# Performance work log

Measured on AMD Instinct MI355X. Metric: run time of the kernel, lower is better.

## Reference

```python
import jax, jax.numpy as jnp
from jax import lax
import numpy as np

THRESHOLD = 1.25
CURRENT_DECAY = 0.25
VOLTAGE_DECAY = 0.03
TAU_GRAD = 0.03
SCALE_GRAD = 3.0


@jax.custom_vjp
def spike_fn(v):
    # Heaviside spike on membrane voltage (threshold already subtracted)
    return (v >= 0.0).astype(v.dtype)

def _spike_fwd(v):
    return spike_fn(v), v

def _spike_bwd(v, g):
    # slayer-style exponential surrogate gradient around threshold
    surrogate = SCALE_GRAD * jnp.exp(-jnp.abs(v) / TAU_GRAD)
    return (g * surrogate,)

spike_fn.defvjp(_spike_fwd, _spike_bwd)


def cuba_dense(x, v_w, g_w, delay):
    """x: [B, C_in, T] spikes -> [B, C_out, T] spikes.
    Weight-normalized dense synapse + CUBA leaky-integrate-and-fire scan + axonal delay."""
    # weight norm: W = g * v / ||v||_row
    norm = jnp.sqrt(jnp.sum(v_w * v_w, axis=1, keepdims=True))
    W = g_w[:, None] * v_w / norm                       # [O, C]
    z = jnp.einsum('bct,oc->bot', x, W)                 # synaptic current input [B, O, T]
    B, O, T = z.shape
    zT = jnp.transpose(z, (2, 0, 1))                    # [T, B, O]

    def step(carry, zt):
        cur, vol = carry
        cur = cur * (1.0 - CURRENT_DECAY) + zt
        vol = vol * (1.0 - VOLTAGE_DECAY) + cur
        s = spike_fn(vol - THRESHOLD)
        vol = vol * (1.0 - s)                           # reset to zero on spike
        return (cur, vol), s

    init = (jnp.zeros((B, O), z.dtype), jnp.zeros((B, O), z.dtype))
    _, sT = lax.scan(step, init, zT)                    # [T, B, O]
    s = jnp.transpose(sT, (1, 2, 0))                    # [B, O, T]

    # per-neuron integer axonal delay: out[b,n,t] = s[b,n,t-d_n]
    t_idx = jnp.arange(T)[None, :] - delay[:, None]     # [O, T]
    valid = (t_idx >= 0)
    gathered = s[:, jnp.arange(O)[:, None], jnp.clip(t_idx, 0, T - 1)]
    return jnp.where(valid[None, :, :], gathered, jnp.zeros((), s.dtype))


def setup_inputs() -> dict:
    key = jax.random.key(0)
    ks = jax.random.split(key, 10)
    B, C, T = 32, 34 * 34 * 2, 300
    spike = (jax.random.uniform(ks[0], (B, C, T)) < 0.1).astype(jnp.float32)
    v1 = jax.random.normal(ks[1], (512, C), jnp.float32) * 0.1
    g1 = jax.random.uniform(ks[2], (512,), jnp.float32) + 0.5
    v2 = jax.random.normal(ks[3], (512, 512), jnp.float32) * 0.1
    g2 = jax.random.uniform(ks[4], (512,), jnp.float32) + 0.5
    v3 = jax.random.normal(ks[5], (10, 512), jnp.float32) * 0.1
    g3 = jax.random.uniform(ks[6], (10,), jnp.float32) + 0.5
    d1 = jax.random.randint(ks[7], (512,), 0, 8, jnp.int32)
    d2 = jax.random.randint(ks[8], (512,), 0, 8, jnp.int32)
    d3 = jax.random.randint(ks[9], (10,), 0, 8, jnp.int32)
    return {"spike": spike, "v1": v1, "g1": g1, "v2": v2, "g2": g2,
            "v3": v3, "g3": g3, "d1": d1, "d2": d2, "d3": d3}


def reference(spike, v1, g1, v2, g2, v3, g3, d1, d2, d3):
    s1 = cuba_dense(spike, v1, g1, d1)
    s2 = cuba_dense(s1, v2, g2, d2)
    s3 = cuba_dense(s2, v3, g3, d3)
    counts = jnp.stack([jnp.mean(s1), jnp.mean(s2), jnp.mean(s3)]).reshape(1, -1)
    return s3, counts
```

## Files before the change

kernel.cpp:

```cpp
#include <hip/hip_runtime.h>

#define B_   32
#define T_   300
#define C1_  2312
#define O1_  512
#define O2_  512
#define O3_  10
#define M_   (B_*T_)
#define KSPLIT_ 1152


__global__ void calc_f(const float* __restrict__ v, const float* __restrict__ g,
                       double* __restrict__ f, int O, int C) {
    int o = blockIdx.x;
    const float* row = v + (size_t)o * C;
    double s = 0.0;
    for (int c = threadIdx.x; c < C; c += blockDim.x) {
        double x = (double)row[c];
        s += x * x;
    }
    for (int off = 32; off; off >>= 1) s += __shfl_down(s, off);
    __shared__ double wsum[4];
    int lane = threadIdx.x & 63, wv = threadIdx.x >> 6;
    if (lane == 0) wsum[wv] = s;
    __syncthreads();
    if (threadIdx.x == 0) {
        double tot = 0.0;
        for (int i = 0; i < (int)(blockDim.x >> 6); ++i) tot += wsum[i];
        f[o] = (double)g[o] / sqrt(tot);
    }
}

__global__ void transpose_scale(const float* __restrict__ v, const double* __restrict__ f,
                                double* __restrict__ wt, int O, int C, int ldo) {
    __shared__ double tile[32][33];
    int c0 = blockIdx.x * 32, o0 = blockIdx.y * 32;
    int tx = threadIdx.x, ty = threadIdx.y;
    for (int k = 0; k < 4; ++k) {
        int o = o0 + ty + k * 8, c = c0 + tx;
        double val = 0.0;
        if (o < O && c < C) val = (double)v[(size_t)o * C + c] * f[o];
        tile[ty + k * 8][tx] = val;
    }
    __syncthreads();
    for (int k = 0; k < 4; ++k) {
        int c = c0 + ty + k * 8, o = o0 + tx;
        if (c < C && o < O) wt[(size_t)c * ldo + o] = tile[tx][ty + k * 8];
    }
}

__global__ void build_bits(const float* __restrict__ X, unsigned* __restrict__ bits) {
    size_t idx = (size_t)blockIdx.x * 256 + threadIdx.x;
    if (idx >= (size_t)B_ * C1_ * 10) return;
    int t32 = (int)(idx % 10);
    size_t bc = idx / 10;
    const float* src = X + bc * T_ + t32 * 32;
    int nq = (t32 == 9) ? 3 : 8;
    unsigned m = 0;
    for (int q = 0; q < nq; ++q) {
        float4 v = *(const float4*)(src + q * 4);
        if (v.x != 0.f) m |= 1u << (q * 4 + 0);
        if (v.y != 0.f) m |= 1u << (q * 4 + 1);
        if (v.z != 0.f) m |= 1u << (q * 4 + 2);
        if (v.w != 0.f) m |= 1u << (q * 4 + 3);
    }
    bits[idx] = m;
}

__global__ __launch_bounds__(512, 4) void gemm1(const unsigned* __restrict__ Xbits,
                                                const double* __restrict__ Wt,
                                                double* __restrict__ Z0,
                                                double* __restrict__ Z1) {
    __shared__ double Ws[2][16][256];
    int n = blockIdx.x;
    int combo = n & 3;
    int khalf = combo & 1;
    int o0 = (combo >> 1) * 256;
    int i = n >> 2;
    int tb = i % 10;
    int bpair = i / 10;
    int tid = threadIdx.x;
    int w = tid >> 6;
    int lane = tid & 63;
    int b = bpair * 2 + (w >> 2);
    int w8s = __builtin_amdgcn_readfirstlane((w & 3) << 3);
    int cbeg = khalf ? KSPLIT_ : 0;
    int qend = khalf ? C1_ : KSPLIT_;
    const int NT = khalf ? 73 : 72;
    double* __restrict__ Z = khalf ? Z1 : Z0;
    double acc[8][4];
#pragma unroll
    for (int tj = 0; tj < 8; ++tj)
#pragma unroll
        for (int i2 = 0; i2 < 4; ++i2) acc[tj][i2] = 0.0;
    const unsigned* xbp = Xbits + (size_t)b * C1_ * 10 + tb;

    double2 wreg[4];
    unsigned mval, mvaln = 0u;

    auto load_w = [&](int c0) {
#pragma unroll
        for (int h = 0; h < 4; ++h) {
            int idx = h * 512 + tid;
            int r = idx >> 7, od = (idx & 127) * 2;
            int c = c0 + r;
            double2 val; val.x = 0.0; val.y = 0.0;
            if (c < qend) val = *(const double2*)(Wt + (size_t)c * O1_ + o0 + od);
            wreg[h] = val;
        }
    };
    auto load_m = [&](int c0) -> unsigned {
        int c = c0 + lane;
        return (lane < 16 && c < qend) ? xbp[(size_t)c * 10] : 0u;
    };
    auto store_w = [&](int bi) {
#pragma unroll
        for (int h = 0; h < 4; ++h) {
            int idx = h * 512 + tid;
            int r = idx >> 7, od = (idx & 127) * 2;
            *(double2*)(&Ws[bi][r][od]) = wreg[h];
        }
    };

    load_w(cbeg);
    mval = load_m(cbeg);
    store_w(0);
    __syncthreads();
    int cur = 0;
    for (int tile = 0; tile < NT; ++tile) {
        if (tile + 1 < NT) {
            int cn = cbeg + (tile + 1) * 16;
            load_w(cn);
            mvaln = load_m(cn);
        }
#pragma unroll
        for (int k = 0; k < 16; ++k) {
            unsigned smk = (unsigned)__builtin_amdgcn_readlane((int)mval, k);
            unsigned soct = (smk >> w8s) & 0xffu;
            if (soct) {
                double wf[4];
#pragma unroll
                for (int i2 = 0; i2 < 4; ++i2) wf[i2] = Ws[cur][k][lane + 64 * i2];
#pragma unroll
                for (int tj = 0; tj < 8; ++tj) {
                    if (soct & (1u << tj)) {
#pragma unroll
                        for (int i2 = 0; i2 < 4; ++i2) acc[tj][i2] += wf[i2];
                    }
                }
            }
        }
        if (tile + 1 < NT) {
            store_w(cur ^ 1);
            __syncthreads();
        }
        mval = mvaln;
        cur ^= 1;
    }
#pragma unroll
    for (int tj = 0; tj < 8; ++tj) {
        int t = tb * 32 + w8s + tj;
        if (t < T_) {
            double* dst = Z + ((size_t)b * T_ + t) * O1_ + o0;
#pragma unroll
            for (int i2 = 0; i2 < 4; ++i2)
                dst[lane + 64 * i2] = acc[tj][i2];
        }
    }
}

__global__ __launch_bounds__(512, 4) void gemm2s(const unsigned* __restrict__ Sbits,
                                                 const double* __restrict__ Wt,
                                                 double* __restrict__ Z0,
                                                 double* __restrict__ Z1) {
    __shared__ double Ws[2][16][256];
    int n = blockIdx.x;
    int combo = n & 3;
    int khalf = combo & 1;
    int o0 = (combo >> 1) * 256;
    int i = n >> 2;
    int twin = i % 5;
    int b = i / 5;
    int tid = threadIdx.x;
    int w = tid >> 6;
    int lane = tid & 63;
    int w8s = __builtin_amdgcn_readfirstlane((w & 3) << 3);
    int word = twin * 2 + (w >> 2);
    int cbeg = khalf * 256;
    double* __restrict__ Z = khalf ? Z1 : Z0;
    double acc[8][4];
#pragma unroll
    for (int tj = 0; tj < 8; ++tj)
#pragma unroll
        for (int i2 = 0; i2 < 4; ++i2) acc[tj][i2] = 0.0;
    const unsigned* xbp = Sbits + (size_t)b * O1_ * 10 + word;

    double2 wreg[4];
    unsigned mval, mvaln = 0u;

    auto load_w = [&](int c0) {
#pragma unroll
        for (int h = 0; h < 4; ++h) {
            int idx = h * 512 + tid;
            int r = idx >> 7, od = (idx & 127) * 2;
            int c = c0 + r;
            wreg[h] = *(const double2*)(Wt + (size_t)c * O2_ + o0 + od);
        }
    };
    auto load_m = [&](int c0) -> unsigned {
        int c = c0 + lane;
        return (lane < 16) ? xbp[(size_t)c * 10] : 0u;
    };
    auto store_w = [&](int bi) {
#pragma unroll
        for (int h = 0; h < 4; ++h) {
            int idx = h * 512 + tid;
            int r = idx >> 7, od = (idx & 127) * 2;
            *(double2*)(&Ws[bi][r][od]) = wreg[h];
        }
    };

    load_w(cbeg);
    mval = load_m(cbeg);
    store_w(0);
    __syncthreads();
    int cur = 0;
    for (int tile = 0; tile < 16; ++tile) {
        if (tile + 1 < 16) {
            int cn = cbeg + (tile + 1) * 16;
            load_w(cn);
            mvaln = load_m(cn);
        }
#pragma unroll
        for (int k = 0; k < 16; ++k) {
            unsigned smk = (unsigned)__builtin_amdgcn_readlane((int)mval, k);
            unsigned soct = (smk >> w8s) & 0xffu;
            if (soct) {
                double wf[4];
#pragma unroll
                for (int i2 = 0; i2 < 4; ++i2) wf[i2] = Ws[cur][k][lane + 64 * i2];
#pragma unroll
                for (int tj = 0; tj < 8; ++tj) {
                    if (soct & (1u << tj)) {
#pragma unroll
                        for (int i2 = 0; i2 < 4; ++i2) acc[tj][i2] += wf[i2];
                    }
                }
            }
        }
        if (tile + 1 < 16) {
            store_w(cur ^ 1);
            __syncthreads();
        }
        mval = mvaln;
        cur ^= 1;
    }
#pragma unroll
    for (int tj = 0; tj < 8; ++tj) {
        int t = twin * 64 + w * 8 + tj;
        if (t < T_) {
            double* dst = Z + ((size_t)b * T_ + t) * O2_ + o0;
#pragma unroll
            for (int i2 = 0; i2 < 4; ++i2)
                dst[lane + 64 * i2] = acc[tj][i2];
        }
    }
}

__global__ void gemm3(const float* __restrict__ A,
                      const double* __restrict__ Wt,
                      double* __restrict__ Z) {
    __shared__ double w[512 * 16];
    for (int e = threadIdx.x; e < 4096; e += 256)
        ((double2*)w)[e] = ((const double2*)Wt)[e];
    __syncthreads();
    int m = blockIdx.x * 256 + threadIdx.x;
    if (m >= M_) return;
    double acc[O3_];
#pragma unroll
    for (int o = 0; o < O3_; ++o) acc[o] = 0.0;
    const float4* Ar = (const float4*)(A + (size_t)m * 512);
    for (int cq = 0; cq < 128; ++cq) {
        float4 a = Ar[cq];
        float av[4] = {a.x, a.y, a.z, a.w};
#pragma unroll
        for (int u = 0; u < 4; ++u)
#pragma unroll
            for (int o = 0; o < O3_; ++o) acc[o] += (double)av[u] * w[(cq * 4 + u) * 16 + o];
    }
    double* dst = Z + (size_t)m * 16;
#pragma unroll
    for (int o = 0; o < O3_; ++o) dst[o] = acc[o];
}

__global__ void scan12(const double* __restrict__ Za,
                       const double* __restrict__ Zb,
                       const int* __restrict__ delay,
                       float* __restrict__ Sout,
                       unsigned* __restrict__ bitsOut,
                       float* __restrict__ sumOut) {
    int blk = blockIdx.x;
    int o = (blk & 7) * 64 + threadIdx.x;
    int b = blk >> 3;
    size_t base = (size_t)b * T_ * O1_ + o;
    const double* z  = Za + base;
    const double* z2 = Zb ? Zb + base : nullptr;
    float* s = Sout ? Sout + base : nullptr;
    int d = delay[o];
    if (s) for (int t = 0; t < d; ++t) s[(size_t)t * O1_] = 0.f;
    double cur = 0.0, vol = 0.0;
    float cnt = 0.f;
    unsigned bw = 0u;
    for (int t8 = 0; t8 < 296; t8 += 8) {
        double zbuf[8];
#pragma unroll
        for (int u = 0; u < 8; ++u) zbuf[u] = z[(size_t)(t8 + u) * O1_];
        if (z2) {
#pragma unroll
            for (int u = 0; u < 8; ++u) zbuf[u] += z2[(size_t)(t8 + u) * O1_];
        }
#pragma unroll
        for (int u = 0; u < 8; ++u) {
            int t = t8 + u;
            cur = cur * 0.75 + zbuf[u];
            vol = vol * 0.97 + cur;
            float sp = (vol >= 1.25) ? 1.f : 0.f;
            if (sp > 0.f) vol = 0.0;
            int tw = t + d;
            if (tw < T_) {
                if (s) s[(size_t)tw * O1_] = sp;
                cnt += sp;
                if (bitsOut) {
                    if (sp > 0.f) bw |= 1u << (tw & 31);
                    if ((tw & 31) == 31) { bitsOut[((size_t)b * O1_ + o) * 10 + (tw >> 5)] = bw; bw = 0u; }
                }
            }
        }
    }
    {
        double zbuf[4];
#pragma unroll
        for (int u = 0; u < 4; ++u) zbuf[u] = z[(size_t)(296 + u) * O1_];
        if (z2) {
#pragma unroll
            for (int u = 0; u < 4; ++u) zbuf[u] += z2[(size_t)(296 + u) * O1_];
        }
#pragma unroll
        for (int u = 0; u < 4; ++u) {
            int t = 296 + u;
            cur = cur * 0.75 + zbuf[u];
            vol = vol * 0.97 + cur;
            float sp = (vol >= 1.25) ? 1.f : 0.f;
            if (sp > 0.f) vol = 0.0;
            int tw = t + d;
            if (tw < T_) {
                if (s) s[(size_t)tw * O1_] = sp;
                cnt += sp;
                if (bitsOut) {
                    if (sp > 0.f) bw |= 1u << (tw & 31);
                    if ((tw & 31) == 31) { bitsOut[((size_t)b * O1_ + o) * 10 + (tw >> 5)] = bw; bw = 0u; }
                }
            }
        }
    }
    if (bitsOut) bitsOut[((size_t)b * O1_ + o) * 10 + 9] = bw;
    for (int off = 32; off; off >>= 1) cnt += __shfl_down(cnt, off);
    if (threadIdx.x == 0) atomicAdd(sumOut, cnt);
}

__global__ void scan3(const double* __restrict__ Z3,
                      const int* __restrict__ d3,
                      float* __restrict__ out,
                      float* __restrict__ sumOut) {
    __shared__ double zt[T_ * 16];
    int b = blockIdx.x;
    const double2* src = (const double2*)(Z3 + (size_t)b * T_ * 16);
    for (int e = threadIdx.x; e < T_ * 8; e += 64)
        ((double2*)zt)[e] = src[e];
    __syncthreads();
    int o = threadIdx.x;
    if (o < O3_) {
        int d = d3[o];
        float* dst = out + (size_t)b * O3_ * T_ + (size_t)o * T_;
        for (int t = 0; t < d; ++t) dst[t] = 0.f;
        double cur = 0.0, vol = 0.0;
        float cnt = 0.f;
        for (int t = 0; t < T_; ++t) {
            cur = cur * 0.75 + zt[t * 16 + o];
            vol = vol * 0.97 + cur;
            float sp = (vol >= 1.25) ? 1.f : 0.f;
            if (sp > 0.f) vol = 0.0;
            int tw = t + d;
            if (tw < T_) { dst[tw] = sp; cnt += sp; }
        }
        atomicAdd(sumOut, cnt);
    }
}

__global__ void finalize(const float* __restrict__ sums, float* __restrict__ out) {
    if (threadIdx.x == 0) {
        out[0] = (float)((double)sums[0] / (double)(B_ * O1_ * T_));
        out[1] = (float)((double)sums[1] / (double)(B_ * O2_ * T_));
        out[2] = (float)((double)sums[2] / (double)(B_ * O3_ * T_));
    }
}

extern "C" void kernel_launch(void* const* d_in, const int* in_sizes, int n_in,
                              void* d_out, int out_size, void* d_ws, size_t ws_size,
                              hipStream_t stream) {
    const float* spike = (const float*)d_in[0];
    const float* v1 = (const float*)d_in[1];
    const float* g1 = (const float*)d_in[2];
    const float* v2 = (const float*)d_in[3];
    const float* g2 = (const float*)d_in[4];
    const float* v3 = (const float*)d_in[5];
    const float* g3 = (const float*)d_in[6];
    const int* d1 = (const int*)d_in[7];
    const int* d2 = (const int*)d_in[8];
    const int* d3 = (const int*)d_in[9];
    float* out = (float*)d_out;

    double* dw = (double*)d_ws;
    size_t off = 0;
    double* f1  = dw + off; off += 512;
    double* f2  = dw + off; off += 512;
    double* f3  = dw + off; off += 16;
    double* Wt1 = dw + off; off += (size_t)C1_ * O1_;
    double* Wt2 = dw + off; off += 512 * 512;
    double* Wt3 = dw + off; off += 512 * 16;
    double* zA  = dw + off; off += (size_t)M_ * 512;
    double* zB  = dw + off; off += (size_t)M_ * 512;
    double* z3b = dw + off; off += (size_t)M_ * 16;
    float* fw = (float*)(dw + off);
    float* sB    = fw;
    float* sums  = fw + (size_t)M_ * 512;
    unsigned* Xbits = (unsigned*)(fw + (size_t)M_ * 512 + 4);
    unsigned* bits2 = Xbits + (size_t)B_ * C1_ * 10;
    (void)ws_size; (void)out_size; (void)in_sizes; (void)n_in;

    hipMemsetAsync(sums, 0, 4 * sizeof(float), stream);

    build_bits<<<(B_ * C1_ * 10 + 255) / 256, 256, 0, stream>>>(spike, Xbits);

    calc_f<<<512, 256, 0, stream>>>(v1, g1, f1, O1_, C1_);
    calc_f<<<512, 256, 0, stream>>>(v2, g2, f2, O2_, O1_);
    calc_f<<<O3_, 256, 0, stream>>>(v3, g3, f3, O3_, O2_);

    transpose_scale<<<dim3((C1_ + 31) / 32, 16), dim3(32, 8), 0, stream>>>(v1, f1, Wt1, O1_, C1_, O1_);
    transpose_scale<<<dim3(16, 16), dim3(32, 8), 0, stream>>>(v2, f2, Wt2, O2_, O1_, O2_);
    transpose_scale<<<dim3(16, 1), dim3(32, 8), 0, stream>>>(v3, f3, Wt3, O3_, O2_, 16);

    gemm1<<<640, 512, 0, stream>>>(Xbits, Wt1, zA, zB);
    scan12<<<256, 64, 0, stream>>>(zA, zB, d1, nullptr, bits2, sums + 0);
    gemm2s<<<640, 512, 0, stream>>>(bits2, Wt2, zA, zB);
    scan12<<<256, 64, 0, stream>>>(zA, zB, d2, sB, nullptr, sums + 1);
    gemm3<<<(M_ + 255) / 256, 256, 0, stream>>>(sB, Wt3, z3b);
    scan3<<<B_, 64, 0, stream>>>(z3b, d3, out, sums + 2);
    finalize<<<1, 64, 0, stream>>>(sums, out + (size_t)B_ * O3_ * T_);
}
```

Before: 794.1 us.

## Replace bit-packed sparse gemm2 with dense FP64 tiled FMA GEMM

Layer-2 GEMM previously used bit-packed spike masks and conditionally added weight rows only for active spikes, split over two K-halves. It now reads float spikes written by scan12 and runs a dense 32x128 tiled FP64 FMA GEMM over the full K. This removes the bit-packing, branch divergence and the second partial-sum buffer, but does full dense FP64 work regardless of spike sparsity. scan12 is now called with a null second buffer, so it must handle that case.

```diff
diff --git a/kernel.cpp b/kernel.cpp
--- a/kernel.cpp
+++ b/kernel.cpp
@@ -169,101 +169,53 @@
     }
 }
 
-__global__ __launch_bounds__(512, 4) void gemm2s(const unsigned* __restrict__ Sbits,
-                                                 const double* __restrict__ Wt,
-                                                 double* __restrict__ Z0,
-                                                 double* __restrict__ Z1) {
-    __shared__ double Ws[2][16][256];
-    int n = blockIdx.x;
-    int combo = n & 3;
-    int khalf = combo & 1;
-    int o0 = (combo >> 1) * 256;
-    int i = n >> 2;
-    int twin = i % 5;
-    int b = i / 5;
+__global__ __launch_bounds__(256, 4) void gemm2(const float* __restrict__ A,
+                                                const double* __restrict__ Wt,
+                                                double* __restrict__ Z) {
+    __shared__ double Ws[16][128];
+    __shared__ float  As[32][20];
+    int m0 = blockIdx.x * 32;
+    int o0 = blockIdx.y * 128;
     int tid = threadIdx.x;
-    int w = tid >> 6;
-    int lane = tid & 63;
-    int w8s = __builtin_amdgcn_readfirstlane((w & 3) << 3);
-    int word = twin * 2 + (w >> 2);
-    int cbeg = khalf * 256;
-    double* __restrict__ Z = khalf ? Z1 : Z0;
-    double acc[8][4];
-#pragma unroll
-    for (int tj = 0; tj < 8; ++tj)
-#pragma unroll
-        for (int i2 = 0; i2 < 4; ++i2) acc[tj][i2] = 0.0;
-    const unsigned* xbp = Sbits + (size_t)b * O1_ * 10 + word;
-
-    double2 wreg[4];
-    unsigned mval, mvaln = 0u;
-
-    auto load_w = [&](int c0) {
+    int to = tid & 31, tm = tid >> 5;
+    double acc[4][4];
+#pragma unroll
+    for (int i = 0; i < 4; ++i)
+#pragma unroll
+        for (int j = 0; j < 4; ++j) acc[i][j] = 0.0;
+    for (int c0 = 0; c0 < 512; c0 += 16) {
+        {
+            int r = tid >> 3, pr = tid & 7;
+            float2 v = *(const float2*)(A + (size_t)(m0 + r) * 512 + c0 + pr * 2);
+            As[r][pr * 2 + 0] = v.x;
+            As[r][pr * 2 + 1] = v.y;
+        }
 #pragma unroll
         for (int h = 0; h < 4; ++h) {
-            int idx = h * 512 + tid;
-            int r = idx >> 7, od = (idx & 127) * 2;
-            int c = c0 + r;
-            wreg[h] = *(const double2*)(Wt + (size_t)c * O2_ + o0 + od);
-        }
-    };
-    auto load_m = [&](int c0) -> unsigned {
-        int c = c0 + lane;
-        return (lane < 16) ? xbp[(size_t)c * 10] : 0u;
-    };
-    auto store_w = [&](int bi) {
-#pragma unroll
-        for (int h = 0; h < 4; ++h) {
-            int idx = h * 512 + tid;
-            int r = idx >> 7, od = (idx & 127) * 2;
-            *(double2*)(&Ws[bi][r][od]) = wreg[h];
-        }
-    };
-
-    load_w(cbeg);
-    mval = load_m(cbeg);
-    store_w(0);
-    __syncthreads();
-    int cur = 0;
-    for (int tile = 0; tile < 16; ++tile) {
-        if (tile + 1 < 16) {
-            int cn = cbeg + (tile + 1) * 16;
-            load_w(cn);
-            mvaln = load_m(cn);
-        }
+            int idx = h * 512 + tid * 2;
+            int k = idx >> 7, o = idx & 127;
+            *(double2*)(&Ws[k][o]) = *(const double2*)(Wt + (size_t)(c0 + k) * O2_ + o0 + o);
+        }
+        __syncthreads();
 #pragma unroll
         for (int k = 0; k < 16; ++k) {
-            unsigned smk = (unsigned)__builtin_amdgcn_readlane((int)mval, k);
-            unsigned soct = (smk >> w8s) & 0xffu;
-            if (soct) {
-                double wf[4];
-#pragma unroll
-                for (int i2 = 0; i2 < 4; ++i2) wf[i2] = Ws[cur][k][lane + 64 * i2];
-#pragma unroll
-                for (int tj = 0; tj < 8; ++tj) {
-                    if (soct & (1u << tj)) {
-#pragma unroll
-                        for (int i2 = 0; i2 < 4; ++i2) acc[tj][i2] += wf[i2];
-                    }
-                }
-            }
-        }
-        if (tile + 1 < 16) {
-            store_w(cur ^ 1);
-            __syncthreads();
-        }
-        mval = mvaln;
-        cur ^= 1;
-    }
-#pragma unroll
-    for (int tj = 0; tj < 8; ++tj) {
-        int t = twin * 64 + w * 8 + tj;
-        if (t < T_) {
-            double* dst = Z + ((size_t)b * T_ + t) * O2_ + o0;
-#pragma unroll
-            for (int i2 = 0; i2 < 4; ++i2)
-                dst[lane + 64 * i2] = acc[tj][i2];
-        }
+            double wf[4], xf[4];
+#pragma unroll
+            for (int i = 0; i < 4; ++i) wf[i] = Ws[k][to + 32 * i];
+#pragma unroll
+            for (int j = 0; j < 4; ++j) xf[j] = (double)As[tm * 4 + j][k];
+#pragma unroll
+            for (int i = 0; i < 4; ++i)
+#pragma unroll
+                for (int j = 0; j < 4; ++j) acc[i][j] = fma(wf[i], xf[j], acc[i][j]);
+        }
+        __syncthreads();
+    }
+#pragma unroll
+    for (int j = 0; j < 4; ++j) {
+        double* dst = Z + (size_t)(m0 + tm * 4 + j) * O2_ + o0;
+#pragma unroll
+        for (int i = 0; i < 4; ++i) dst[to + 32 * i] = acc[i][j];
     }
 }
 
@@ -435,7 +387,6 @@
     float* sB    = fw;
     float* sums  = fw + (size_t)M_ * 512;
     unsigned* Xbits = (unsigned*)(fw + (size_t)M_ * 512 + 4);
-    unsigned* bits2 = Xbits + (size_t)B_ * C1_ * 10;
     (void)ws_size; (void)out_size; (void)in_sizes; (void)n_in;
 
     hipMemsetAsync(sums, 0, 4 * sizeof(float), stream);
@@ -451,9 +402,9 @@
     transpose_scale<<<dim3(16, 1), dim3(32, 8), 0, stream>>>(v3, f3, Wt3, O3_, O2_, 16);
 
     gemm1<<<640, 512, 0, stream>>>(Xbits, Wt1, zA, zB);
-    scan12<<<256, 64, 0, stream>>>(zA, zB, d1, nullptr, bits2, sums + 0);
-    gemm2s<<<640, 512, 0, stream>>>(bits2, Wt2, zA, zB);
-    scan12<<<256, 64, 0, stream>>>(zA, zB, d2, sB, nullptr, sums + 1);
+    scan12<<<256, 64, 0, stream>>>(zA, zB, d1, sB, nullptr, sums + 0);
+    gemm2<<<dim3(300, 4), 256, 0, stream>>>(sB, Wt2, zA);
+    scan12<<<256, 64, 0, stream>>>(zA, nullptr, d2, sB, nullptr, sums + 1);
     gemm3<<<(M_ + 255) / 256, 256, 0, stream>>>(sB, Wt3, z3b);
     scan3<<<B_, 64, 0, stream>>>(z3b, d3, out, sums + 2);
     finalize<<<1, 64, 0, stream>>>(sums, out + (size_t)B_ * O3_ * T_);
```

Result: no change. 794.9 us (+0.1%).
